# Performance work log

Hardware: AMD Instinct MI355X
Metric: run time of the kernel (lower is better)

Reference implementation:

```python
import jax, jax.numpy as jnp
import numpy as np

D_MODEL = 256

def setup_inputs() -> dict:
    key = jax.random.key(0)
    ks = jax.random.split(key, 6)
    B, Tx, Tm, D = 4, 512, 512, D_MODEL
    s = 1.0 / np.sqrt(D)
    return {
        "x": jax.random.normal(ks[0], (B, Tx, D), jnp.float32),
        "memory": jax.random.normal(ks[1], (B, Tm, D), jnp.float32),
        "memory_mask": jnp.ones((B, Tm), jnp.int32),
        "ws1_w": jax.random.uniform(ks[2], (D, D), jnp.float32, -s, s),
        "ws1_b": jax.random.uniform(ks[3], (D,), jnp.float32, -s, s),
        "ws2_w": jax.random.uniform(ks[4], (D, D), jnp.float32, -s, s),
        "wst_w": jax.random.uniform(ks[5], (D,), jnp.float32, -s, s),
    }

def reference(x, memory, memory_mask, ws1_w, ws1_b, ws2_w, wst_w):
    # item1: [B,Tx,D], item2: [B,Tm,D]  (torch Linear: y = x @ W^T + b)
    item1 = jnp.einsum("bxd,ed->bxe", x, ws1_w) + ws1_b
    item2 = jnp.einsum("bmd,ed->bme", memory, ws2_w)
    # broadcast add -> [B,Tx,Tm,D], tanh, reduce by wst -> scores [B,Tx,Tm]
    item = jnp.tanh(item1[:, :, None, :] + item2[:, None, :, :])
    S = jnp.einsum("bxmd,d->bxm", item, wst_w)
    S = jnp.where(memory_mask[:, None, :] == 0, -jnp.inf, S)
    S = jax.nn.softmax(S, axis=-1)
    out = jnp.einsum("bxm,bmd->bxd", S, memory)
    return (out, S)
```

## Files before the change

### kernel.cpp

```cpp
#include <hip/hip_runtime.h>

#define D_MODEL 256
#define TX 512
#define TM 512

__device__ __forceinline__ float fexp2(float x) { return __builtin_amdgcn_exp2f(x); }
__device__ __forceinline__ float frcp(float x)  { return __builtin_amdgcn_rcpf(x); }

__device__ __forceinline__ float quad(float4 a, float4 e, float4 w, float acc) {
    float p1 = fmaf(a.x, e.x, 1.f);
    float p2 = fmaf(a.y, e.y, 1.f);
    float p3 = fmaf(a.z, e.z, 1.f);
    float p4 = fmaf(a.w, e.w, 1.f);
    float p12 = p1 * p2;
    float p34 = p3 * p4;
    float q12 = fmaf(w.x, p2, w.y * p1);
    float q34 = fmaf(w.z, p4, w.w * p3);
    float N   = fmaf(q12, p34, q34 * p12);
    float D   = p12 * p34;
    return fmaf(N, frcp(D), acc);
}

__global__ __launch_bounds__(128) void gemm_exp2(
    const float* __restrict__ x,   const float* __restrict__ mem,
    const float* __restrict__ w1,  const float* __restrict__ b1,
    const float* __restrict__ w2,
    float* __restrict__ E1, float* __restrict__ E2p)
{
    const float C_SCALE = 2.8853900817779268f;
    const int bid = (int)blockIdx.x;
    const float* A; const float* W;
    int r0, n0;
    if (blockIdx.z == 0) { A = x;  W = w1; r0 = (bid & 63) * 32; n0 = (bid >> 6) * 64; }
    else                 { A = w2; W = mem; r0 = (bid & 7) * 32;  n0 = (bid >> 3) * 64; }

    __shared__ float As[2][16][36];
    __shared__ float Ws[2][16][68];
    const int tid = threadIdx.x;
    const int tx = tid & 15, ty = tid >> 4;
    const int rl = tid >> 2, g = tid & 3;
    float acc[4][4] = {};
    const float* Ap  = A + (size_t)(r0 + rl) * 256 + g * 4;
    const float* Wp0 = W + (size_t)(n0 + rl) * 256 + g * 4;
    const float* Wp1 = W + (size_t)(n0 + 32 + rl) * 256 + g * 4;

    {
        float4 a4 = *(const float4*)Ap;
        float4 w4 = *(const float4*)Wp0;
        float4 w5 = *(const float4*)Wp1;
        As[0][g*4+0][rl] = a4.x; As[0][g*4+1][rl] = a4.y;
        As[0][g*4+2][rl] = a4.z; As[0][g*4+3][rl] = a4.w;
        Ws[0][g*4+0][rl] = w4.x; Ws[0][g*4+1][rl] = w4.y;
        Ws[0][g*4+2][rl] = w4.z; Ws[0][g*4+3][rl] = w4.w;
        Ws[0][g*4+0][rl+32] = w5.x; Ws[0][g*4+1][rl+32] = w5.y;
        Ws[0][g*4+2][rl+32] = w5.z; Ws[0][g*4+3][rl+32] = w5.w;
    }
    __syncthreads();

    for (int k0 = 0; k0 < 16; ++k0) {
        const int cur = k0 & 1;
        float4 an, wn, vn;
        if (k0 < 15) {
            an = *(const float4*)(Ap  + (k0 + 1) * 16);
            wn = *(const float4*)(Wp0 + (k0 + 1) * 16);
            vn = *(const float4*)(Wp1 + (k0 + 1) * 16);
        }
        #pragma unroll
        for (int kk = 0; kk < 16; ++kk) {
            float4 av = *(const float4*)&As[cur][kk][ty*4];
            float4 wv = *(const float4*)&Ws[cur][kk][tx*4];
            float a_[4] = {av.x, av.y, av.z, av.w};
            float w_[4] = {wv.x, wv.y, wv.z, wv.w};
            #pragma unroll
            for (int i = 0; i < 4; ++i)
                #pragma unroll
                for (int j = 0; j < 4; ++j)
                    acc[i][j] = fmaf(a_[i], w_[j], acc[i][j]);
        }
        if (k0 < 15) {
            const int nxt = cur ^ 1;
            As[nxt][g*4+0][rl] = an.x; As[nxt][g*4+1][rl] = an.y;
            As[nxt][g*4+2][rl] = an.z; As[nxt][g*4+3][rl] = an.w;
            Ws[nxt][g*4+0][rl] = wn.x; Ws[nxt][g*4+1][rl] = wn.y;
            Ws[nxt][g*4+2][rl] = wn.z; Ws[nxt][g*4+3][rl] = wn.w;
            Ws[nxt][g*4+0][rl+32] = vn.x; Ws[nxt][g*4+1][rl+32] = vn.y;
            Ws[nxt][g*4+2][rl+32] = vn.z; Ws[nxt][g*4+3][rl+32] = vn.w;
            __syncthreads();
        }
    }

    if (blockIdx.z == 0) {
        #pragma unroll
        for (int i = 0; i < 4; ++i) {
            const int r = r0 + ty*4 + i;
            #pragma unroll
            for (int j = 0; j < 4; ++j) {
                const int n = n0 + tx*4 + j;
                E1[(size_t)r*256 + n] = fexp2(C_SCALE * (acc[i][j] + b1[n]));
            }
        }
    } else {
        #pragma unroll
        for (int i = 0; i < 4; ++i) {
            const int r = r0 + ty*4 + i;
            #pragma unroll
            for (int j = 0; j < 4; ++j) {
                const int n = n0 + tx*4 + j;
                E2p[(size_t)(r >> 2)*8192 + (size_t)n*4 + (r & 3)] = fexp2(C_SCALE * acc[i][j]);
            }
        }
    }
}

__global__ __launch_bounds__(512) void fused_tanh_attn(
    const float* __restrict__ E1,
    const float* __restrict__ E2p,
    const float* __restrict__ memory,
    const int*   __restrict__ mask,
    const float* __restrict__ wst,
    float* __restrict__ out,
    float* __restrict__ Sout)
{
    const float LOG2E = 1.4426950408889634f;
    const int t = threadIdx.x;
    const int blk = (int)((blockIdx.x & 7) * 64 + (blockIdx.x >> 3));
    const int b = blk >> 7;
    const int x0 = (blk & 127) * 4;
    const int wave = t >> 6, lane = t & 63;
    const int tm = t & 255;
    const int dh = t >> 8;

    __shared__ float i1R[4][D_MODEL];
    __shared__ float wsh[D_MODEL];
    __shared__ float Pa[4][TM];
    __shared__ float Pb[4][TM];
    __shared__ float mneg[TM];
    __shared__ float opart[8][4][D_MODEL];
    __shared__ float wpart[8];
    __shared__ float smax[4][2], ssum[4][2];

    {
        const float* i1g = E1 + ((size_t)b * TX + x0) * D_MODEL;
        const int row = t >> 7, col2 = (t & 127) * 2;
        float2 v = *(const float2*)(i1g + (size_t)row * D_MODEL + col2);
        *(float2*)&i1R[row][col2] = v;
    }
    if (t < 256) wsh[t] = wst[t];
    mneg[t] = mask[b*TM + t] ? 0.f : -__builtin_inff();

    {
        float s = (t < 256) ? wst[t] : 0.f;
        #pragma unroll
        for (int off = 32; off > 0; off >>= 1) s += __shfl_xor(s, off);
        if (lane == 0) wpart[wave] = s;
    }

    const int g0 = dh * 32;
    const float* e2ptrA = E2p + ((size_t)b * TM + tm) * 4;
    const float* e2ptrB = e2ptrA + 1024;
    float4 e2a = *(const float4*)(e2ptrA + (size_t)g0 * 8192);
    float4 e2b = *(const float4*)(e2ptrB + (size_t)g0 * 8192);

    __syncthreads();
    const float Wsum = wpart[0] + wpart[1] + wpart[2] + wpart[3]
                     + wpart[4] + wpart[5] + wpart[6] + wpart[7];

    float accA[4] = {}, accB[4] = {};
    #pragma unroll 2
    for (int gi = 0; gi < 32; ++gi) {
        const int g = g0 + gi;
        float4 e2an = e2a, e2bn = e2b;
        if (gi < 31) {
            e2an = *(const float4*)(e2ptrA + (size_t)(g + 1) * 8192);
            e2bn = *(const float4*)(e2ptrB + (size_t)(g + 1) * 8192);
        }
        float4 w4 = *(const float4*)&wsh[g * 4];
        #pragma unroll
        for (int r = 0; r < 4; ++r) {
            float4 a = *(const float4*)&i1R[r][g * 4];
            accA[r] = quad(a, e2a, w4, accA[r]);
            accB[r] = quad(a, e2b, w4, accB[r]);
        }
        e2a = e2an; e2b = e2bn;
    }

    if (dh == 0) {
        #pragma unroll
        for (int r = 0; r < 4; ++r) { Pa[r][tm] = accA[r]; Pa[r][tm + 256] = accB[r]; }
    } else {
        #pragma unroll
        for (int r = 0; r < 4; ++r) { Pb[r][tm] = accA[r]; Pb[r][tm + 256] = accB[r]; }
    }
    __syncthreads();

    {
        const int r = wave & 3, h = wave >> 2;
        const int base = h * 256 + lane * 4;
        float4 va = *(const float4*)&Pa[r][base];
        float4 vb = *(const float4*)&Pb[r][base];
        float4 mn = *(const float4*)&mneg[base];
        float v0 = Wsum - 2.f * (va.x + vb.x) + mn.x;
        float v1 = Wsum - 2.f * (va.y + vb.y) + mn.y;
        float v2 = Wsum - 2.f * (va.z + vb.z) + mn.z;
        float v3 = Wsum - 2.f * (va.w + vb.w) + mn.w;
        float mx = fmaxf(fmaxf(v0, v1), fmaxf(v2, v3));
        #pragma unroll
        for (int off = 32; off > 0; off >>= 1) mx = fmaxf(mx, __shfl_xor(mx, off));
        float e0 = fexp2((v0 - mx) * LOG2E);
        float e1 = fexp2((v1 - mx) * LOG2E);
        float e2 = fexp2((v2 - mx) * LOG2E);
        float e3 = fexp2((v3 - mx) * LOG2E);
        float sum = (e0 + e1) + (e2 + e3);
        #pragma unroll
        for (int off = 32; off > 0; off >>= 1) sum += __shfl_xor(sum, off);
        if (lane == 0) { smax[r][h] = mx; ssum[r][h] = sum; }
        __syncthreads();
        const float m0 = smax[r][0], m1 = smax[r][1];
        const float mg = fmaxf(m0, m1);
        const float tot = ssum[r][0] * fexp2((m0 - mg) * LOG2E)
                        + ssum[r][1] * fexp2((m1 - mg) * LOG2E);
        const float fac = fexp2((mx - mg) * LOG2E) * frcp(tot);
        float4 p = {e0 * fac, e1 * fac, e2 * fac, e3 * fac};
        *(float4*)&Pa[r][base] = p;
        *(float4*)(Sout + ((size_t)b*TX + x0 + r) * TM + base) = p;
    }
    __syncthreads();

    {
        const int m0 = wave * 64;
        const float* memp = memory + ((size_t)b * TM + m0) * D_MODEL + lane * 4;
        float4 o0 = {0,0,0,0}, o1 = {0,0,0,0}, o2 = {0,0,0,0}, o3 = {0,0,0,0};
        float4 mvA[4], mvB[4];
        #pragma unroll
        for (int j = 0; j < 4; ++j) mvA[j] = *(const float4*)(memp + (size_t)j * D_MODEL);
        #pragma unroll
        for (int j = 0; j < 4; ++j) mvB[j] = *(const float4*)(memp + (size_t)(4 + j) * D_MODEL);
        #pragma unroll
        for (int c = 0; c < 16; ++c) {
            float4 p0 = *(const float4*)&Pa[0][m0 + c*4];
            float4 p1 = *(const float4*)&Pa[1][m0 + c*4];
            float4 p2 = *(const float4*)&Pa[2][m0 + c*4];
            float4 p3 = *(const float4*)&Pa[3][m0 + c*4];
            #pragma unroll
            for (int j = 0; j < 4; ++j) {
                float4 mv = (c & 1) ? mvB[j] : mvA[j];
                if (c < 14) {
                    float4 nf = *(const float4*)(memp + (size_t)((c + 2) * 4 + j) * D_MODEL);
                    if (c & 1) mvB[j] = nf; else mvA[j] = nf;
                }
                const float q0 = (j==0)?p0.x:(j==1)?p0.y:(j==2)?p0.z:p0.w;
                const float q1 = (j==0)?p1.x:(j==1)?p1.y:(j==2)?p1.z:p1.w;
                const float q2 = (j==0)?p2.x:(j==1)?p2.y:(j==2)?p2.z:p2.w;
                const float q3 = (j==0)?p3.x:(j==1)?p3.y:(j==2)?p3.z:p3.w;
                o0.x = fmaf(q0, mv.x, o0.x); o0.y = fmaf(q0, mv.y, o0.y);
                o0.z = fmaf(q0, mv.z, o0.z); o0.w = fmaf(q0, mv.w, o0.w);
                o1.x = fmaf(q1, mv.x, o1.x); o1.y = fmaf(q1, mv.y, o1.y);
                o1.z = fmaf(q1, mv.z, o1.z); o1.w = fmaf(q1, mv.w, o1.w);
                o2.x = fmaf(q2, mv.x, o2.x); o2.y = fmaf(q2, mv.y, o2.y);
                o2.z = fmaf(q2, mv.z, o2.z); o2.w = fmaf(q2, mv.w, o2.w);
                o3.x = fmaf(q3, mv.x, o3.x); o3.y = fmaf(q3, mv.y, o3.y);
                o3.z = fmaf(q3, mv.z, o3.z); o3.w = fmaf(q3, mv.w, o3.w);
            }
        }
        *(float4*)&opart[wave][0][lane*4] = o0;
        *(float4*)&opart[wave][1][lane*4] = o1;
        *(float4*)&opart[wave][2][lane*4] = o2;
        *(float4*)&opart[wave][3][lane*4] = o3;
    }
    __syncthreads();

    {
        #pragma unroll
        for (int k = 0; k < 2; ++k) {
            const int idx = t + k * 512;
            const int row = idx >> 8, d0 = idx & 255;
            float s = 0.f;
            #pragma unroll
            for (int w = 0; w < 8; ++w) s += opart[w][row][d0];
            out[((size_t)b*TX + x0 + row) * D_MODEL + d0] = s;
        }
    }
}

extern "C" void kernel_launch(void* const* d_in, const int* in_sizes, int n_in,
                              void* d_out, int out_size, void* d_ws, size_t ws_size,
                              hipStream_t stream) {
    const float* x    = (const float*)d_in[0];
    const float* mem  = (const float*)d_in[1];
    const int*   mask = (const int*)d_in[2];
    const float* w1   = (const float*)d_in[3];
    const float* b1   = (const float*)d_in[4];
    const float* w2   = (const float*)d_in[5];
    const float* wst  = (const float*)d_in[6];

    float* out  = (float*)d_out;
    float* Sout = out + 4 * 512 * 256;
    float* E1   = (float*)d_ws;
    float* E2p  = E1 + 4 * 512 * 256;

    dim3 gg(256, 1, 2);
    gemm_exp2<<<gg, 128, 0, stream>>>(x, mem, w1, b1, w2, E1, E2p);
    fused_tanh_attn<<<512, 512, 0, stream>>>(E1, E2p, mem, mask, wst, out, Sout);
}
```

Measured before the change: 64.61 us.

## Double block size to 1024 threads, splitting the D reduction four ways

The fused attention kernel now launches 1024 threads per block instead of 512. Each thread covers a quarter of the feature dimension rather than half, and the partial scores are combined across four shared-memory slices. The softmax uses 16 waves with 2 elements per lane and a four-way max/sum merge. The P·memory stage gives each wave 32 memory rows, drops the register double-buffered prefetch, and adds an extra shared-memory pass to fold waves 8-15 into waves 0-7. This is meant to raise parallelism and latency hiding, at the cost of more synchronisation, tighter register limits under launch_bounds(1024,8), and loss of the explicit load prefetch.

```diff
diff --git a/kernel.cpp b/kernel.cpp
--- a/kernel.cpp
+++ b/kernel.cpp
@@ -112,7 +112,7 @@
     }
 }
 
-__global__ __launch_bounds__(512) void fused_tanh_attn(
+__global__ __launch_bounds__(1024, 8) void fused_tanh_attn(
     const float* __restrict__ E1,
     const float* __restrict__ E2p,
     const float* __restrict__ memory,
@@ -128,49 +128,45 @@
     const int x0 = (blk & 127) * 4;
     const int wave = t >> 6, lane = t & 63;
     const int tm = t & 255;
-    const int dh = t >> 8;
+    const int dq = t >> 8;
 
     __shared__ float i1R[4][D_MODEL];
     __shared__ float wsh[D_MODEL];
-    __shared__ float Pa[4][TM];
-    __shared__ float Pb[4][TM];
+    __shared__ float Pq[4][4][TM];
     __shared__ float mneg[TM];
     __shared__ float opart[8][4][D_MODEL];
-    __shared__ float wpart[8];
-    __shared__ float smax[4][2], ssum[4][2];
+    __shared__ float wpart[4];
+    __shared__ float smax[4][4], ssum[4][4];
 
     {
         const float* i1g = E1 + ((size_t)b * TX + x0) * D_MODEL;
-        const int row = t >> 7, col2 = (t & 127) * 2;
-        float2 v = *(const float2*)(i1g + (size_t)row * D_MODEL + col2);
-        *(float2*)&i1R[row][col2] = v;
+        i1R[t >> 8][t & 255] = i1g[(size_t)(t >> 8) * D_MODEL + (t & 255)];
     }
     if (t < 256) wsh[t] = wst[t];
-    mneg[t] = mask[b*TM + t] ? 0.f : -__builtin_inff();
-
-    {
-        float s = (t < 256) ? wst[t] : 0.f;
+    if (t < 512) mneg[t] = mask[b*TM + t] ? 0.f : -__builtin_inff();
+
+    if (wave < 4) {
+        float s = wst[wave * 64 + lane];
         #pragma unroll
         for (int off = 32; off > 0; off >>= 1) s += __shfl_xor(s, off);
         if (lane == 0) wpart[wave] = s;
     }
 
-    const int g0 = dh * 32;
+    const int g0 = dq * 16;
     const float* e2ptrA = E2p + ((size_t)b * TM + tm) * 4;
     const float* e2ptrB = e2ptrA + 1024;
     float4 e2a = *(const float4*)(e2ptrA + (size_t)g0 * 8192);
     float4 e2b = *(const float4*)(e2ptrB + (size_t)g0 * 8192);
 
     __syncthreads();
-    const float Wsum = wpart[0] + wpart[1] + wpart[2] + wpart[3]
-                     + wpart[4] + wpart[5] + wpart[6] + wpart[7];
+    const float Wsum = wpart[0] + wpart[1] + wpart[2] + wpart[3];
 
     float accA[4] = {}, accB[4] = {};
     #pragma unroll 2
-    for (int gi = 0; gi < 32; ++gi) {
+    for (int gi = 0; gi < 16; ++gi) {
         const int g = g0 + gi;
         float4 e2an = e2a, e2bn = e2b;
-        if (gi < 31) {
+        if (gi < 15) {
             e2an = *(const float4*)(e2ptrA + (size_t)(g + 1) * 8192);
             e2bn = *(const float4*)(e2ptrB + (size_t)(g + 1) * 8192);
         }
@@ -184,70 +180,59 @@
         e2a = e2an; e2b = e2bn;
     }
 
-    if (dh == 0) {
-        #pragma unroll
-        for (int r = 0; r < 4; ++r) { Pa[r][tm] = accA[r]; Pa[r][tm + 256] = accB[r]; }
-    } else {
-        #pragma unroll
-        for (int r = 0; r < 4; ++r) { Pb[r][tm] = accA[r]; Pb[r][tm + 256] = accB[r]; }
-    }
-    __syncthreads();
-
-    {
-        const int r = wave & 3, h = wave >> 2;
-        const int base = h * 256 + lane * 4;
-        float4 va = *(const float4*)&Pa[r][base];
-        float4 vb = *(const float4*)&Pb[r][base];
-        float4 mn = *(const float4*)&mneg[base];
-        float v0 = Wsum - 2.f * (va.x + vb.x) + mn.x;
-        float v1 = Wsum - 2.f * (va.y + vb.y) + mn.y;
-        float v2 = Wsum - 2.f * (va.z + vb.z) + mn.z;
-        float v3 = Wsum - 2.f * (va.w + vb.w) + mn.w;
-        float mx = fmaxf(fmaxf(v0, v1), fmaxf(v2, v3));
+    #pragma unroll
+    for (int r = 0; r < 4; ++r) {
+        Pq[dq][r][tm]       = accA[r];
+        Pq[dq][r][tm + 256] = accB[r];
+    }
+    __syncthreads();
+
+    {
+        const int r = wave & 3, qq = wave >> 2;
+        const int m = qq * 128 + lane * 2;
+        float2 a0 = *(const float2*)&Pq[0][r][m];
+        float2 a1 = *(const float2*)&Pq[1][r][m];
+        float2 a2 = *(const float2*)&Pq[2][r][m];
+        float2 a3 = *(const float2*)&Pq[3][r][m];
+        float2 mn = *(const float2*)&mneg[m];
+        float v0 = Wsum - 2.f * ((a0.x + a1.x) + (a2.x + a3.x)) + mn.x;
+        float v1 = Wsum - 2.f * ((a0.y + a1.y) + (a2.y + a3.y)) + mn.y;
+        float mx = fmaxf(v0, v1);
         #pragma unroll
         for (int off = 32; off > 0; off >>= 1) mx = fmaxf(mx, __shfl_xor(mx, off));
         float e0 = fexp2((v0 - mx) * LOG2E);
         float e1 = fexp2((v1 - mx) * LOG2E);
-        float e2 = fexp2((v2 - mx) * LOG2E);
-        float e3 = fexp2((v3 - mx) * LOG2E);
-        float sum = (e0 + e1) + (e2 + e3);
+        float sum = e0 + e1;
         #pragma unroll
         for (int off = 32; off > 0; off >>= 1) sum += __shfl_xor(sum, off);
-        if (lane == 0) { smax[r][h] = mx; ssum[r][h] = sum; }
+        if (lane == 0) { smax[r][qq] = mx; ssum[r][qq] = sum; }
         __syncthreads();
-        const float m0 = smax[r][0], m1 = smax[r][1];
-        const float mg = fmaxf(m0, m1);
+        const float m0 = smax[r][0], m1 = smax[r][1], m2 = smax[r][2], m3 = smax[r][3];
+        const float mg = fmaxf(fmaxf(m0, m1), fmaxf(m2, m3));
         const float tot = ssum[r][0] * fexp2((m0 - mg) * LOG2E)
-                        + ssum[r][1] * fexp2((m1 - mg) * LOG2E);
+                        + ssum[r][1] * fexp2((m1 - mg) * LOG2E)
+                        + ssum[r][2] * fexp2((m2 - mg) * LOG2E)
+                        + ssum[r][3] * fexp2((m3 - mg) * LOG2E);
         const float fac = fexp2((mx - mg) * LOG2E) * frcp(tot);
-        float4 p = {e0 * fac, e1 * fac, e2 * fac, e3 * fac};
-        *(float4*)&Pa[r][base] = p;
-        *(float4*)(Sout + ((size_t)b*TX + x0 + r) * TM + base) = p;
-    }
-    __syncthreads();
-
-    {
-        const int m0 = wave * 64;
+        float2 p = {e0 * fac, e1 * fac};
+        *(float2*)&Pq[0][r][m] = p;
+        *(float2*)(Sout + ((size_t)b*TX + x0 + r) * TM + m) = p;
+    }
+    __syncthreads();
+
+    float4 o0 = {0,0,0,0}, o1 = {0,0,0,0}, o2 = {0,0,0,0}, o3 = {0,0,0,0};
+    {
+        const int m0 = wave * 32;
         const float* memp = memory + ((size_t)b * TM + m0) * D_MODEL + lane * 4;
-        float4 o0 = {0,0,0,0}, o1 = {0,0,0,0}, o2 = {0,0,0,0}, o3 = {0,0,0,0};
-        float4 mvA[4], mvB[4];
-        #pragma unroll
-        for (int j = 0; j < 4; ++j) mvA[j] = *(const float4*)(memp + (size_t)j * D_MODEL);
-        #pragma unroll
-        for (int j = 0; j < 4; ++j) mvB[j] = *(const float4*)(memp + (size_t)(4 + j) * D_MODEL);
-        #pragma unroll
-        for (int c = 0; c < 16; ++c) {
-            float4 p0 = *(const float4*)&Pa[0][m0 + c*4];
-            float4 p1 = *(const float4*)&Pa[1][m0 + c*4];
-            float4 p2 = *(const float4*)&Pa[2][m0 + c*4];
-            float4 p3 = *(const float4*)&Pa[3][m0 + c*4];
+        #pragma unroll
+        for (int c = 0; c < 8; ++c) {
+            float4 p0 = *(const float4*)&Pq[0][0][m0 + c*4];
+            float4 p1 = *(const float4*)&Pq[0][1][m0 + c*4];
+            float4 p2 = *(const float4*)&Pq[0][2][m0 + c*4];
+            float4 p3 = *(const float4*)&Pq[0][3][m0 + c*4];
             #pragma unroll
             for (int j = 0; j < 4; ++j) {
-                float4 mv = (c & 1) ? mvB[j] : mvA[j];
-                if (c < 14) {
-                    float4 nf = *(const float4*)(memp + (size_t)((c + 2) * 4 + j) * D_MODEL);
-                    if (c & 1) mvB[j] = nf; else mvA[j] = nf;
-                }
+                float4 mv = *(const float4*)(memp + (size_t)(c*4 + j) * D_MODEL);
                 const float q0 = (j==0)?p0.x:(j==1)?p0.y:(j==2)?p0.z:p0.w;
                 const float q1 = (j==0)?p1.x:(j==1)?p1.y:(j==2)?p1.z:p1.w;
                 const float q2 = (j==0)?p2.x:(j==1)?p2.y:(j==2)?p2.z:p2.w;
@@ -262,23 +247,37 @@
                 o3.z = fmaf(q3, mv.z, o3.z); o3.w = fmaf(q3, mv.w, o3.w);
             }
         }
+    }
+    if (wave < 8) {
         *(float4*)&opart[wave][0][lane*4] = o0;
         *(float4*)&opart[wave][1][lane*4] = o1;
         *(float4*)&opart[wave][2][lane*4] = o2;
         *(float4*)&opart[wave][3][lane*4] = o3;
     }
     __syncthreads();
-
-    {
-        #pragma unroll
-        for (int k = 0; k < 2; ++k) {
-            const int idx = t + k * 512;
-            const int row = idx >> 8, d0 = idx & 255;
-            float s = 0.f;
-            #pragma unroll
-            for (int w = 0; w < 8; ++w) s += opart[w][row][d0];
-            out[((size_t)b*TX + x0 + row) * D_MODEL + d0] = s;
-        }
+    if (wave >= 8) {
+        const int w2 = wave - 8;
+        float4 u0 = *(const float4*)&opart[w2][0][lane*4];
+        float4 u1 = *(const float4*)&opart[w2][1][lane*4];
+        float4 u2 = *(const float4*)&opart[w2][2][lane*4];
+        float4 u3 = *(const float4*)&opart[w2][3][lane*4];
+        u0.x += o0.x; u0.y += o0.y; u0.z += o0.z; u0.w += o0.w;
+        u1.x += o1.x; u1.y += o1.y; u1.z += o1.z; u1.w += o1.w;
+        u2.x += o2.x; u2.y += o2.y; u2.z += o2.z; u2.w += o2.w;
+        u3.x += o3.x; u3.y += o3.y; u3.z += o3.z; u3.w += o3.w;
+        *(float4*)&opart[w2][0][lane*4] = u0;
+        *(float4*)&opart[w2][1][lane*4] = u1;
+        *(float4*)&opart[w2][2][lane*4] = u2;
+        *(float4*)&opart[w2][3][lane*4] = u3;
+    }
+    __syncthreads();
+
+    {
+        const int row = t >> 8, d0 = t & 255;
+        float s = 0.f;
+        #pragma unroll
+        for (int w = 0; w < 8; ++w) s += opart[w][row][d0];
+        out[((size_t)b*TX + x0 + row) * D_MODEL + d0] = s;
     }
 }
 
@@ -300,5 +299,5 @@
 
     dim3 gg(256, 1, 2);
     gemm_exp2<<<gg, 128, 0, stream>>>(x, mem, w1, b1, w2, E1, E2p);
-    fused_tanh_attn<<<512, 512, 0, stream>>>(E1, E2p, mem, mask, wst, out, Sout);
+    fused_tanh_attn<<<512, 1024, 0, stream>>>(E1, E2p, mem, mask, wst, out, Sout);
 }
```

New measurement: 76.46 us. 1.18x slower.
